# Optimization experiments

Hardware: AMD Instinct MI355X
Metric: run time of the kernel (lower is better)

## Reference

```python
import jax, jax.numpy as jnp
import numpy as np

B, L, D, H, NB = 8, 256, 128, 4, 2
HD = D // H
N_ITEMS, TIME_SPAN = 50000, 256
EPS = 1e-8
NEG = -(2.0 ** 32) + 1.0  # torch uses -2**32+1 padding value


def _ln(x, g, b):
    m = jnp.mean(x, -1, keepdims=True)
    v = jnp.mean((x - m) ** 2, -1, keepdims=True)
    return (x - m) / jnp.sqrt(v + EPS) * g + b


def setup_inputs() -> dict:
    ks = iter(jax.random.split(jax.random.key(0), 40))

    def nrm(shape, s=0.02):
        return jax.random.normal(next(ks), shape, jnp.float32) * s

    inp = {
        "user_ids": jax.random.randint(next(ks), (B,), 0, 1000),
        "log_seqs": jax.random.randint(next(ks), (B, L), 0, N_ITEMS + 1),
        "time_matrices": jax.random.randint(next(ks), (B, L, L), 0, TIME_SPAN + 1),
        "pos_seqs": jax.random.randint(next(ks), (B, L), 1, N_ITEMS + 1),
        "neg_seqs": jax.random.randint(next(ks), (B, L), 1, N_ITEMS + 1),
    }
    inp["item_emb"] = nrm((N_ITEMS + 1, D)).at[0].set(0.0)  # padding_idx=0
    inp["posK_emb"] = nrm((L, D))
    inp["posV_emb"] = nrm((L, D))
    inp["timeK_emb"] = nrm((TIME_SPAN + 1, D))
    inp["timeV_emb"] = nrm((TIME_SPAN + 1, D))
    inp["ln1_g"] = jnp.ones((NB, D)); inp["ln1_b"] = jnp.zeros((NB, D))
    inp["Wq"] = nrm((NB, D, D)); inp["bq"] = jnp.zeros((NB, D))
    inp["Wk"] = nrm((NB, D, D)); inp["bk"] = jnp.zeros((NB, D))
    inp["Wv"] = nrm((NB, D, D)); inp["bv"] = jnp.zeros((NB, D))
    inp["ln2_g"] = jnp.ones((NB, D)); inp["ln2_b"] = jnp.zeros((NB, D))
    inp["W1"] = nrm((NB, D, D)); inp["b1"] = jnp.zeros((NB, D))
    inp["W2"] = nrm((NB, D, D)); inp["b2"] = jnp.zeros((NB, D))
    inp["lnf_g"] = jnp.ones((D,)); inp["lnf_b"] = jnp.zeros((D,))
    return inp


def reference(user_ids, log_seqs, time_matrices, pos_seqs, neg_seqs,
              item_emb, posK_emb, posV_emb, timeK_emb, timeV_emb,
              ln1_g, ln1_b, Wq, bq, Wk, bk, Wv, bv, ln2_g, ln2_b,
              W1, b1, W2, b2, lnf_g, lnf_b):
    # dropout layers are identity in eval mode
    seqs = item_emb[log_seqs] * jnp.sqrt(jnp.float32(D))          # [B,L,D]
    tK = timeK_emb[time_matrices].reshape(B, L, L, H, HD)          # [B,Lq,Lk,H,hd]
    tV = timeV_emb[time_matrices].reshape(B, L, L, H, HD)
    pad = log_seqs == 0                                            # [B,L]
    seqs = seqs * (~pad)[..., None]
    causal = jnp.triu(jnp.ones((L, L), bool), 1)                   # ~tril -> masked
    # time_mask masks by QUERY position (matches torch unsqueeze(-1).expand)
    mask = pad[:, None, :, None] | causal[None, None]              # [B,1,Lq,Lk]
    posKh = posK_emb.reshape(L, H, HD)
    posVh = posV_emb.reshape(L, H, HD)
    for i in range(NB):
        q_in = _ln(seqs, ln1_g[i], ln1_b[i])
        Qh = (q_in @ Wq[i] + bq[i]).reshape(B, L, H, HD).transpose(0, 2, 1, 3)
        Kh = (seqs @ Wk[i] + bk[i]).reshape(B, L, H, HD).transpose(0, 2, 1, 3)
        Vh = (seqs @ Wv[i] + bv[i]).reshape(B, L, H, HD).transpose(0, 2, 1, 3)
        scores = jnp.einsum("bhqd,bhkd->bhqk", Qh, Kh)
        scores = scores + jnp.einsum("bhqd,khd->bhqk", Qh, posKh)
        scores = scores + jnp.einsum("bqkhd,bhqd->bhqk", tK, Qh)
        scores = scores / jnp.sqrt(jnp.float32(HD))
        scores = jnp.where(mask, NEG, scores)
        A = jax.nn.softmax(scores, axis=-1)                        # [B,H,Lq,Lk]
        out = jnp.einsum("bhqk,bhkd->bhqd", A, Vh)
        out = out + jnp.einsum("bhqk,khd->bhqd", A, posVh)
        out = out + jnp.einsum("bhqk,bqkhd->bhqd", A, tV)
        out = out.transpose(0, 2, 1, 3).reshape(B, L, D)
        seqs = q_in + out                                          # residual on Q
        seqs = _ln(seqs, ln2_g[i], ln2_b[i])
        h = jax.nn.relu(seqs @ W1[i] + b1[i])                      # conv1d k=1 == linear
        seqs = seqs + (h @ W2[i] + b2[i])
        seqs = seqs * (~pad)[..., None]
    feats = _ln(seqs, lnf_g, lnf_b)
    pos_logits = jnp.sum(feats * item_emb[pos_seqs], -1)           # [B,L]
    neg_logits = jnp.sum(feats * item_emb[neg_seqs], -1)
    return (pos_logits, neg_logits)
```

## Files before the change

kernel.cpp:

```cpp
#include <hip/hip_runtime.h>
#include <hip/hip_bf16.h>

#define L_ 256
#define H_ 4
#define ROWS 2048
#define NEGV (-4294967295.0f)

typedef unsigned short us16;

__device__ __forceinline__ float us2f(us16 u){ return __uint_as_float(((unsigned)u)<<16); }
__device__ __forceinline__ us16 f2us(float f){ __hip_bfloat16 h=__float2bfloat16(f); return *(us16*)&h; }

__device__ __forceinline__ float dot2bf(unsigned x, unsigned y, float c){
#if __has_builtin(__builtin_amdgcn_fdot2_f32_bf16)
    typedef __bf16 bf2 __attribute__((ext_vector_type(2)));
    union U{ unsigned u; bf2 v; };
    U ux, uy; ux.u=x; uy.u=y;
    return __builtin_amdgcn_fdot2_f32_bf16(ux.v, uy.v, c, false);
#else
    float r=fmaf(us2f((us16)(x&0xffffu)), us2f((us16)(y&0xffffu)), c);
    return fmaf(us2f((us16)(x>>16)), us2f((us16)(y>>16)), r);
#endif
}

struct KArgs {
    const int *log_seqs, *tmat, *pos_seqs, *neg_seqs;
    const float *item_emb, *posK, *posV, *timeK, *timeV;
    const float *ln1g, *ln1b, *bq, *bk, *bv, *ln2g, *ln2b, *b1, *b2, *lnfg, *lnfb;
    const float *Wq, *Wk, *Wv, *W1, *W2;
    float *qin0, *qin1, *out;
    unsigned *wsP;
    us16 *tmK, *tmV, *Qb0, *Kb0, *Vb0, *Qb1, *Kb1, *Vb1;
};

struct __align__(16) Smem {
    float    sS[8*256];
    float    sPr[16*128];
    float    sPj[2*257*4];
    unsigned sAb[8*128];
    int      sTM[512];
    unsigned sQb[128];
    float    sX[256];
    unsigned sXb[128];
    unsigned sHb[128];
    unsigned sYb[128];
    float    sRed[4], sRed2[4], sRB[8];
};

__device__ __forceinline__ float gemv128(const unsigned* __restrict__ wcol,
                                         const unsigned* __restrict__ xp){
    const uint4* w4=(const uint4*)wcol;
    const uint4* x4=(const uint4*)xp;
    float s0=0.f,s1=0.f,s2=0.f,s3=0.f;
    #pragma unroll
    for(int j=0;j<16;j++){
        uint4 w=w4[j], x=x4[j];
        s0=dot2bf(x.x,w.x,s0); s1=dot2bf(x.y,w.y,s1);
        s2=dot2bf(x.z,w.z,s2); s3=dot2bf(x.w,w.w,s3);
    }
    return (s0+s1)+(s2+s3);
}

__device__ __forceinline__ void ln_rows(float* sA,
        const float* __restrict__ g, const float* __restrict__ b,
        float* qin_out, int r0, int tid){
    int r=tid>>5, l=tid&31;
    float* x=sA+r*128;
    float x0=x[l],x1=x[l+32],x2=x[l+64],x3=x[l+96];
    float s=x0+x1+x2+x3;
    #pragma unroll
    for(int o=16;o;o>>=1) s+=__shfl_xor(s,o,64);
    float m=s*(1.f/128.f);
    float d0=x0-m,d1=x1-m,d2=x2-m,d3=x3-m;
    float v=d0*d0+d1*d1+d2*d2+d3*d3;
    #pragma unroll
    for(int o=16;o;o>>=1) v+=__shfl_xor(v,o,64);
    float rstd=rsqrtf(v*(1.f/128.f)+1e-8f);
    float y0=d0*rstd*g[l]+b[l];
    float y1=d1*rstd*g[l+32]+b[l+32];
    float y2=d2*rstd*g[l+64]+b[l+64];
    float y3=d3*rstd*g[l+96]+b[l+96];
    x[l]=y0; x[l+32]=y1; x[l+64]=y2; x[l+96]=y3;
    if(qin_out){
        float* q=qin_out+(size_t)(r0+r)*128;
        q[l]=y0; q[l+32]=y1; q[l+64]=y2; q[l+96]=y3;
    }
}

__global__ __launch_bounds__(256) void k_pre(KArgs a){
    __shared__ __align__(16) float sA[1024];
    int tid=threadIdx.x, bid=blockIdx.x;
    if(bid<768){
        int m=bid>>8, rg=bid&255, r0=rg*8;
        {
            int rl=tid>>5, c4=tid&31;
            int id=a.log_seqs[r0+rl];
            float4 v=((const float4*)a.item_emb)[id*32+c4];
            float sc = id? 11.3137085f : 0.f;
            v.x*=sc; v.y*=sc; v.z*=sc; v.w*=sc;
            ((float4*)sA)[tid]=v;
        }
        __syncthreads();
        if(m==0){ ln_rows(sA, a.ln1g, a.ln1b, a.qin0, r0, tid); __syncthreads(); }
        const float* Wsrc=(m==0)?a.Wq:(m==1)?a.Wk:a.Wv;
        int cp=tid&63, rp=tid>>6, c0=2*cp, ra=2*rp, rb=ra+1;
        float a00=0,a01=0,a10=0,a11=0;
        const float* Ar=sA+ra*128;
        const float* Br=sA+rb*128;
        #pragma unroll 8
        for(int kk=0;kk<128;kk++){
            float2 wp=((const float2*)(Wsrc+(size_t)kk*128))[cp];
            float x0=Ar[kk], x1=Br[kk];
            a00=fmaf(x0,wp.x,a00); a01=fmaf(x0,wp.y,a01);
            a10=fmaf(x1,wp.x,a10); a11=fmaf(x1,wp.y,a11);
        }
        int r_a=r0+ra, r_b=r0+rb;
        if(m==0){
            float b0v=a.bq[c0], b1v=a.bq[c0+1];
            ushort2 s0; s0.x=f2us(a00+b0v); s0.y=f2us(a01+b1v);
            ushort2 s1; s1.x=f2us(a10+b0v); s1.y=f2us(a11+b1v);
            *(ushort2*)(a.Qb0+(size_t)r_a*128+c0)=s0;
            *(ushort2*)(a.Qb0+(size_t)r_b*128+c0)=s1;
        } else if(m==1){
            float b0v=a.bk[c0], b1v=a.bk[c0+1];
            int qa=r_a&255, qb2=r_b&255;
            ushort2 s0; s0.x=f2us(a00+b0v+a.posK[qa*128+c0]);  s0.y=f2us(a01+b1v+a.posK[qa*128+c0+1]);
            ushort2 s1; s1.x=f2us(a10+b0v+a.posK[qb2*128+c0]); s1.y=f2us(a11+b1v+a.posK[qb2*128+c0+1]);
            *(ushort2*)(a.Kb0+(size_t)r_a*128+c0)=s0;
            *(ushort2*)(a.Kb0+(size_t)r_b*128+c0)=s1;
        } else {
            float b0v=a.bv[c0], b1v=a.bv[c0+1];
            int qa=r_a&255, qb2=r_b&255;
            unsigned lo0=f2us(a00+b0v+a.posV[qa*128+c0]);
            unsigned lo1=f2us(a01+b1v+a.posV[qa*128+c0+1]);
            unsigned hi0=f2us(a10+b0v+a.posV[qb2*128+c0]);
            unsigned hi1=f2us(a11+b1v+a.posV[qb2*128+c0+1]);
            unsigned* Vo=(unsigned*)a.Vb0+((size_t)r_a>>1)*128;
            Vo[c0]  =lo0|(hi0<<16);
            Vo[c0+1]=lo1|(hi1<<16);
        }
    } else if(bid<880){
        int j=bid-768; int m=j>>4; int sub=j&15;
        const float* base;
        switch(m){
            case 0: base=a.W1; break;        case 1: base=a.W2; break;
            case 2: base=a.Wq+16384; break;  case 3: base=a.Wk+16384; break;
            case 4: base=a.Wv+16384; break;  case 5: base=a.W1+16384; break;
            default: base=a.W2+16384; break;
        }
        unsigned* dst=a.wsP+(size_t)m*8192;
        #pragma unroll
        for(int t2=0;t2<2;t2++){
            int o=sub*512+t2*256+tid;
            int c=o>>6, kp=o&63;
            unsigned lo=f2us(base[(size_t)(2*kp)*128+c]);
            unsigned hi=f2us(base[(size_t)(2*kp+1)*128+c]);
            dst[o]=lo|(hi<<16);
        }
    } else {
        int gi=(bid-880)*256+tid;
        if(gi<8224){
            float4 v=((const float4*)a.timeK)[gi];
            ushort4 o; o.x=f2us(v.x);o.y=f2us(v.y);o.z=f2us(v.z);o.w=f2us(v.w);
            ((ushort4*)a.tmK)[gi]=o;
        } else if(gi<16448){
            int g2=gi-8224;
            float4 v=((const float4*)a.timeV)[g2];
            ushort4 o; o.x=f2us(v.x);o.y=f2us(v.y);o.z=f2us(v.z);o.w=f2us(v.w);
            ((ushort4*)a.tmV)[g2]=o;
        }
    }
}

__global__ __launch_bounds__(256,4) void k_blk(KArgs a, int layer){
    __shared__ Smem sm;
    int tid=threadIdx.x, bid=blockIdx.x;
    int b=bid>>7, p=bid&127;
    int q1=p, q2=255-p, b0=b*L_;
    int r1=b0+q1, r2=b0+q2;
    bool pad1=a.log_seqs[r1]==0, pad2=a.log_seqs[r2]==0;
    const us16* Qb = layer? a.Qb1:a.Qb0;
    const us16* Kb = layer? a.Kb1:a.Kb0;
    const unsigned* Vbu = (const unsigned*)(layer? a.Vb1:a.Vb0);
    const float* qin = layer? a.qin1:a.qin0;
    const float scale=0.17677669529663687f;

    if(tid<128){
        int rowq=tid>>6, j=tid&63;
        int r=rowq?r2:r1;
        sm.sQb[rowq*64+j]=((const unsigned*)Qb)[(size_t)r*64+j];
    }
    sm.sTM[tid]    =a.tmat[(size_t)r1*L_+tid];
    sm.sTM[256+tid]=a.tmat[(size_t)r2*L_+tid];
    __syncthreads();

    for(int t=tid;t<257;t+=256){
        const uint4* T4=(const uint4*)(a.tmK+(size_t)t*128);
        const uint4* Q40=(const uint4*)(sm.sQb);
        const uint4* Q41=(const uint4*)(sm.sQb+64);
        float4 p0v,p1v;
        float* pr0=&p0v.x; float* pr1=&p1v.x;
        #pragma unroll
        for(int h=0;h<4;h++){
            uint4 t0=T4[h*4+0],t1=T4[h*4+1],t2=T4[h*4+2],t3=T4[h*4+3];
            {
                uint4 qa=Q40[h*4+0],qb=Q40[h*4+1],qc=Q40[h*4+2],qd=Q40[h*4+3];
                float s0=0,s1=0;
                s0=dot2bf(qa.x,t0.x,s0); s1=dot2bf(qa.y,t0.y,s1);
                s0=dot2bf(qa.z,t0.z,s0); s1=dot2bf(qa.w,t0.w,s1);
                s0=dot2bf(qb.x,t1.x,s0); s1=dot2bf(qb.y,t1.y,s1);
                s0=dot2bf(qb.z,t1.z,s0); s1=dot2bf(qb.w,t1.w,s1);
                s0=dot2bf(qc.x,t2.x,s0); s1=dot2bf(qc.y,t2.y,s1);
                s0=dot2bf(qc.z,t2.z,s0); s1=dot2bf(qc.w,t2.w,s1);
                s0=dot2bf(qd.x,t3.x,s0); s1=dot2bf(qd.y,t3.y,s1);
                s0=dot2bf(qd.z,t3.z,s0); s1=dot2bf(qd.w,t3.w,s1);
                pr0[h]=s0+s1;
            }
            {
                uint4 qa=Q41[h*4+0],qb=Q41[h*4+1],qc=Q41[h*4+2],qd=Q41[h*4+3];
                float s0=0,s1=0;
                s0=dot2bf(qa.x,t0.x,s0); s1=dot2bf(qa.y,t0.y,s1);
                s0=dot2bf(qa.z,t0.z,s0); s1=dot2bf(qa.w,t0.w,s1);
                s0=dot2bf(qb.x,t1.x,s0); s1=dot2bf(qb.y,t1.y,s1);
                s0=dot2bf(qb.z,t1.z,s0); s1=dot2bf(qb.w,t1.w,s1);
                s0=dot2bf(qc.x,t2.x,s0); s1=dot2bf(qc.y,t2.y,s1);
                s0=dot2bf(qc.z,t2.z,s0); s1=dot2bf(qc.w,t2.w,s1);
                s0=dot2bf(qd.x,t3.x,s0); s1=dot2bf(qd.y,t3.y,s1);
                s0=dot2bf(qd.z,t3.z,s0); s1=dot2bf(qd.w,t3.w,s1);
                pr1[h]=s0+s1;
            }
        }
        ((float4*)sm.sPj)[t]    =p0v;
        ((float4*)sm.sPj)[257+t]=p1v;
    }
    __syncthreads();

    {
        int k=tid;
        const uint4* K4=(const uint4*)(Kb+(size_t)(b0+k)*128);
        #pragma unroll
        for(int i2=0;i2<2;i2++){
            int qq=i2?q2:q1; bool pad=i2?pad2:pad1;
            int tm=sm.sTM[i2*256+k];
            bool act=(k<=qq)&&!pad;
            float o0=NEGV,o1=NEGV,o2=NEGV,o3=NEGV;
            if(act){
                const uint4* Q4=(const uint4*)(sm.sQb+i2*64);
                float4 pj=((const float4*)sm.sPj)[i2*257+tm];
                float r4[4];
                #pragma unroll
                for(int h=0;h<4;h++){
                    uint4 k0=K4[h*4+0],k1=K4[h*4+1],k2=K4[h*4+2],k3=K4[h*4+3];
                    uint4 qa=Q4[h*4+0],qb=Q4[h*4+1],qc=Q4[h*4+2],qd=Q4[h*4+3];
                    float s0=0,s1=0;
                    s0=dot2bf(qa.x,k0.x,s0); s1=dot2bf(qa.y,k0.y,s1);
                    s0=dot2bf(qa.z,k0.z,s0); s1=dot2bf(qa.w,k0.w,s1);
                    s0=dot2bf(qb.x,k1.x,s0); s1=dot2bf(qb.y,k1.y,s1);
                    s0=dot2bf(qb.z,k1.z,s0); s1=dot2bf(qb.w,k1.w,s1);
                    s0=dot2bf(qc.x,k2.x,s0); s1=dot2bf(qc.y,k2.y,s1);
                    s0=dot2bf(qc.z,k2.z,s0); s1=dot2bf(qc.w,k2.w,s1);
                    s0=dot2bf(qd.x,k3.x,s0); s1=dot2bf(qd.y,k3.y,s1);
                    s0=dot2bf(qd.z,k3.z,s0); s1=dot2bf(qd.w,k3.w,s1);
                    r4[h]=s0+s1;
                }
                o0=(r4[0]+pj.x)*scale; o1=(r4[1]+pj.y)*scale;
                o2=(r4[2]+pj.z)*scale; o3=(r4[3]+pj.w)*scale;
            }
            sm.sS[(i2*4+0)*256+k]=o0; sm.sS[(i2*4+1)*256+k]=o1;
            sm.sS[(i2*4+2)*256+k]=o2; sm.sS[(i2*4+3)*256+k]=o3;
        }
    }
    __syncthreads();

    {
        int h=tid>>6, lane=tid&63;
        us16* sab=(us16*)sm.sAb;
        #pragma unroll
        for(int i2=0;i2<2;i2++){
            const float* row=sm.sS+(i2*4+h)*256;
            float v0=row[lane],v1=row[lane+64],v2=row[lane+128],v3=row[lane+192];
            float mm=fmaxf(fmaxf(v0,v1),fmaxf(v2,v3));
            #pragma unroll
            for(int o=32;o;o>>=1) mm=fmaxf(mm,__shfl_xor(mm,o,64));
            float e0=__expf(v0-mm),e1=__expf(v1-mm),e2=__expf(v2-mm),e3=__expf(v3-mm);
            float ss=e0+e1+e2+e3;
            #pragma unroll
            for(int o=32;o;o>>=1) ss+=__shfl_xor(ss,o,64);
            float inv=1.f/ss;
            us16* ar=sab+(i2*4+h)*256;
            ar[lane]    =f2us(e0*inv); ar[lane+64] =f2us(e1*inv);
            ar[lane+128]=f2us(e2*inv); ar[lane+192]=f2us(e3*inv);
        }
    }
    __syncthreads();

    {
        int i2=tid>>7, s8=(tid>>4)&7, dq=tid&15;
        int qq=i2?q2:q1; bool pad=i2?pad2:pad1;
        int kend=pad?L_:qq+1;
        int k0=s8*32;
        int kmax=kend-k0; kmax=kmax<0?0:(kmax>32?32:kmax);
        int npair=(kmax+1)>>1;
        const unsigned* arow=sm.sAb+(i2*4+(dq>>2))*128;
        const int* tmrow=sm.sTM+i2*256;
        float ac0=0,ac1=0,ac2=0,ac3=0,ac4=0,ac5=0,ac6=0,ac7=0;
        for(int kp=0;kp<npair;kp++){
            int kx=k0+2*kp;
            unsigned aa=arow[kx>>1];
            int tma=tmrow[kx], tmb=tmrow[kx+1];
            const uint4* Vp=(const uint4*)(Vbu+((size_t)(b0+kx)>>1)*128+dq*8);
            uint4 va=Vp[0], vb4=Vp[1];
            uint4 ta=((const uint4*)(a.tmV+(size_t)tma*128))[dq];
            uint4 tb=((const uint4*)(a.tmV+(size_t)tmb*128))[dq];
            ac0=dot2bf(aa,va.x,ac0);  ac1=dot2bf(aa,va.y,ac1);
            ac2=dot2bf(aa,va.z,ac2);  ac3=dot2bf(aa,va.w,ac3);
            ac4=dot2bf(aa,vb4.x,ac4); ac5=dot2bf(aa,vb4.y,ac5);
            ac6=dot2bf(aa,vb4.z,ac6); ac7=dot2bf(aa,vb4.w,ac7);
            unsigned p0=__builtin_amdgcn_perm(tb.x,ta.x,0x05040100u);
            unsigned p1=__builtin_amdgcn_perm(tb.x,ta.x,0x07060302u);
            unsigned p2=__builtin_amdgcn_perm(tb.y,ta.y,0x05040100u);
            unsigned p3=__builtin_amdgcn_perm(tb.y,ta.y,0x07060302u);
            unsigned p4=__builtin_amdgcn_perm(tb.z,ta.z,0x05040100u);
            unsigned p5=__builtin_amdgcn_perm(tb.z,ta.z,0x07060302u);
            unsigned p6=__builtin_amdgcn_perm(tb.w,ta.w,0x05040100u);
            unsigned p7=__builtin_amdgcn_perm(tb.w,ta.w,0x07060302u);
            ac0=dot2bf(aa,p0,ac0); ac1=dot2bf(aa,p1,ac1);
            ac2=dot2bf(aa,p2,ac2); ac3=dot2bf(aa,p3,ac3);
            ac4=dot2bf(aa,p4,ac4); ac5=dot2bf(aa,p5,ac5);
            ac6=dot2bf(aa,p6,ac6); ac7=dot2bf(aa,p7,ac7);
        }
        float* dst=sm.sPr+(i2*8+s8)*128+dq*8;
        ((float4*)dst)[0]=make_float4(ac0,ac1,ac2,ac3);
        ((float4*)dst)[1]=make_float4(ac4,ac5,ac6,ac7);
    }
    __syncthreads();

    int ii=tid>>7, l=tid&127;
    bool padown = ii? pad2:pad1;
    int rr = ii? r2:r1;
    int qown = ii? q2:q1;
    {
        float v=qin[(size_t)rr*128+l];
        #pragma unroll
        for(int sl=0;sl<8;sl++) v+=sm.sPr[(ii*8+sl)*128+l];
        float s=v;
        #pragma unroll
        for(int o=32;o;o>>=1) s+=__shfl_xor(s,o,64);
        if((tid&63)==0) sm.sRed[ii*2+((tid>>6)&1)]=s;
        __syncthreads();
        float m=(sm.sRed[ii*2]+sm.sRed[ii*2+1])*(1.f/128.f);
        float d=v-m;
        float vv=d*d;
        #pragma unroll
        for(int o=32;o;o>>=1) vv+=__shfl_xor(vv,o,64);
        if((tid&63)==0) sm.sRed2[ii*2+((tid>>6)&1)]=vv;
        __syncthreads();
        float rstd=rsqrtf((sm.sRed2[ii*2]+sm.sRed2[ii*2+1])*(1.f/128.f)+1e-8f);
        float y=d*rstd*a.ln2g[layer*128+l]+a.ln2b[layer*128+l];
        sm.sX[ii*128+l]=y;
        ((us16*)sm.sXb)[ii*128+l]=f2us(y);
    }
    __syncthreads();

    int cc=l;
    {
        float h1=gemv128(a.wsP+(size_t)(layer?5:0)*8192+(size_t)cc*64, sm.sXb+ii*64);
        h1=fmaxf(h1+a.b1[layer*128+cc],0.f);
        ((us16*)sm.sHb)[ii*128+cc]=f2us(h1);
    }
    __syncthreads();
    float f;
    {
        f=gemv128(a.wsP+(size_t)(layer?6:1)*8192+(size_t)cc*64, sm.sHb+ii*64)
          +a.b2[layer*128+cc]+sm.sX[ii*128+cc];
        if(padown) f=0.f;
    }

    if(layer==0){
        ((us16*)sm.sYb)[ii*128+cc]=f2us(f);
        float s=f;
        #pragma unroll
        for(int o=32;o;o>>=1) s+=__shfl_xor(s,o,64);
        if((tid&63)==0) sm.sRB[ii*2+((tid>>6)&1)]=s;
        __syncthreads();
        float m=(sm.sRB[ii*2]+sm.sRB[ii*2+1])*(1.f/128.f);
        float d=f-m;
        float vv=d*d;
        #pragma unroll
        for(int o=32;o;o>>=1) vv+=__shfl_xor(vv,o,64);
        if((tid&63)==0) sm.sRB[4+ii*2+((tid>>6)&1)]=vv;
        __syncthreads();
        float rstd=rsqrtf((sm.sRB[4+ii*2]+sm.sRB[5+ii*2])*(1.f/128.f)+1e-8f);
        float y1=d*rstd*a.ln1g[128+cc]+a.ln1b[128+cc];
        a.qin1[(size_t)rr*128+cc]=y1;
        ((us16*)sm.sXb)[ii*128+cc]=f2us(y1);
        __syncthreads();
        float accq=gemv128(a.wsP+(size_t)2*8192+(size_t)cc*64, sm.sXb+ii*64)+a.bq[128+cc];
        a.Qb1[(size_t)rr*128+cc]=f2us(accq);
        float acck=gemv128(a.wsP+(size_t)3*8192+(size_t)cc*64, sm.sYb+ii*64)+a.bk[128+cc]+a.posK[qown*128+cc];
        a.Kb1[(size_t)rr*128+cc]=f2us(acck);
        float accv=gemv128(a.wsP+(size_t)4*8192+(size_t)cc*64, sm.sYb+ii*64)+a.bv[128+cc]+a.posV[qown*128+cc];
        ((us16*)a.Vb1)[((size_t)rr>>1)*256+2*cc+(rr&1)]=f2us(accv);
    } else {
        float s=f;
        #pragma unroll
        for(int o=32;o;o>>=1) s+=__shfl_xor(s,o,64);
        if((tid&63)==0) sm.sRB[ii*2+((tid>>6)&1)]=s;
        __syncthreads();
        float m=(sm.sRB[ii*2]+sm.sRB[ii*2+1])*(1.f/128.f);
        float d=f-m;
        float vv=d*d;
        #pragma unroll
        for(int o=32;o;o>>=1) vv+=__shfl_xor(vv,o,64);
        if((tid&63)==0) sm.sRB[4+ii*2+((tid>>6)&1)]=vv;
        __syncthreads();
        float rstd=rsqrtf((sm.sRB[4+ii*2]+sm.sRB[5+ii*2])*(1.f/128.f)+1e-8f);
        sm.sX[ii*128+cc]=d*rstd*a.lnfg[cc]+a.lnfb[cc];
        __syncthreads();
        int w=tid>>6, lane=tid&63;
        int rowi=w>>1, neg=w&1;
        int rg = rowi? r2:r1;
        int id = neg? a.neg_seqs[rg] : a.pos_seqs[rg];
        const float* e=a.item_emb+(size_t)id*128;
        float s2 = sm.sX[rowi*128+lane]*e[lane] + sm.sX[rowi*128+lane+64]*e[lane+64];
        #pragma unroll
        for(int o=32;o;o>>=1) s2+=__shfl_xor(s2,o,64);
        if(lane==0) a.out[neg*ROWS+rg]=s2;
    }
}

extern "C" void kernel_launch(void* const* d_in, const int* in_sizes, int n_in,
                              void* d_out, int out_size, void* d_ws, size_t ws_size,
                              hipStream_t stream) {
    KArgs a;
    a.log_seqs=(const int*)d_in[1];
    a.tmat    =(const int*)d_in[2];
    a.pos_seqs=(const int*)d_in[3];
    a.neg_seqs=(const int*)d_in[4];
    a.item_emb=(const float*)d_in[5];
    a.posK =(const float*)d_in[6];
    a.posV =(const float*)d_in[7];
    a.timeK=(const float*)d_in[8];
    a.timeV=(const float*)d_in[9];
    a.ln1g=(const float*)d_in[10];
    a.ln1b=(const float*)d_in[11];
    a.Wq=(const float*)d_in[12];
    a.bq=(const float*)d_in[13];
    a.Wk=(const float*)d_in[14];
    a.bk=(const float*)d_in[15];
    a.Wv=(const float*)d_in[16];
    a.bv=(const float*)d_in[17];
    a.ln2g=(const float*)d_in[18];
    a.ln2b=(const float*)d_in[19];
    a.W1=(const float*)d_in[20];
    a.b1=(const float*)d_in[21];
    a.W2=(const float*)d_in[22];
    a.b2=(const float*)d_in[23];
    a.lnfg=(const float*)d_in[24];
    a.lnfb=(const float*)d_in[25];

    const size_t MB=1u<<20;
    char* w=(char*)d_ws;
    a.qin0=(float*)(w+0*MB);
    a.qin1=(float*)(w+1*MB);
    a.Qb0 =(us16*) (w+2*MB);
    a.Kb0 =(us16*) (w+2*MB+512*1024);
    a.Vb0 =(us16*) (w+3*MB);
    a.Qb1 =(us16*) (w+3*MB+512*1024);
    a.Kb1 =(us16*) (w+4*MB);
    a.Vb1 =(us16*) (w+4*MB+512*1024);
    a.wsP =(unsigned*)(w+5*MB);
    a.tmK =(us16*) (w+5*MB+256*1024);
    a.tmV =(us16*) (w+5*MB+384*1024);
    a.out =(float*)d_out;

    k_pre<<<946,256,0,stream>>>(a);
    k_blk<<<1024,256,0,stream>>>(a,0);
    k_blk<<<1024,256,0,stream>>>(a,1);
}
```

Measured before the change: 234.7 us.

## Transpose packed weight layout for coalesced GEMV and split time-key projection across lanes

```diff
diff --git a/kernel.cpp b/kernel.cpp
--- a/kernel.cpp
+++ b/kernel.cpp
@@ -47,18 +47,15 @@
     float    sRed[4], sRed2[4], sRB[8];
 };
 
-__device__ __forceinline__ float gemv128(const unsigned* __restrict__ wcol,
-                                         const unsigned* __restrict__ xp){
-    const uint4* w4=(const uint4*)wcol;
-    const uint4* x4=(const uint4*)xp;
-    float s0=0.f,s1=0.f,s2=0.f,s3=0.f;
-    #pragma unroll
-    for(int j=0;j<16;j++){
-        uint4 w=w4[j], x=x4[j];
-        s0=dot2bf(x.x,w.x,s0); s1=dot2bf(x.y,w.y,s1);
-        s2=dot2bf(x.z,w.z,s2); s3=dot2bf(x.w,w.w,s3);
-    }
-    return (s0+s1)+(s2+s3);
+__device__ __forceinline__ float gemv128(const unsigned* __restrict__ wp,
+                                         const unsigned* __restrict__ xp, int c){
+    float s0=0.f, s1=0.f;
+    #pragma unroll 8
+    for(int kp=0;kp<64;kp+=2){
+        s0=dot2bf(xp[kp],   wp[kp*128+c],     s0);
+        s1=dot2bf(xp[kp+1], wp[(kp+1)*128+c], s1);
+    }
+    return s0+s1;
 }
 
 __device__ __forceinline__ void ln_rows(float* sA,
@@ -152,7 +149,7 @@
         #pragma unroll
         for(int t2=0;t2<2;t2++){
             int o=sub*512+t2*256+tid;
-            int c=o>>6, kp=o&63;
+            int kp=o>>7, c=o&127;
             unsigned lo=f2us(base[(size_t)(2*kp)*128+c]);
             unsigned hi=f2us(base[(size_t)(2*kp+1)*128+c]);
             dst[o]=lo|(hi<<16);
@@ -194,44 +191,25 @@
     sm.sTM[256+tid]=a.tmat[(size_t)r2*L_+tid];
     __syncthreads();
 
-    for(int t=tid;t<257;t+=256){
-        const uint4* T4=(const uint4*)(a.tmK+(size_t)t*128);
-        const uint4* Q40=(const uint4*)(sm.sQb);
-        const uint4* Q41=(const uint4*)(sm.sQb+64);
-        float4 p0v,p1v;
-        float* pr0=&p0v.x; float* pr1=&p1v.x;
-        #pragma unroll
-        for(int h=0;h<4;h++){
-            uint4 t0=T4[h*4+0],t1=T4[h*4+1],t2=T4[h*4+2],t3=T4[h*4+3];
-            {
-                uint4 qa=Q40[h*4+0],qb=Q40[h*4+1],qc=Q40[h*4+2],qd=Q40[h*4+3];
-                float s0=0,s1=0;
-                s0=dot2bf(qa.x,t0.x,s0); s1=dot2bf(qa.y,t0.y,s1);
-                s0=dot2bf(qa.z,t0.z,s0); s1=dot2bf(qa.w,t0.w,s1);
-                s0=dot2bf(qb.x,t1.x,s0); s1=dot2bf(qb.y,t1.y,s1);
-                s0=dot2bf(qb.z,t1.z,s0); s1=dot2bf(qb.w,t1.w,s1);
-                s0=dot2bf(qc.x,t2.x,s0); s1=dot2bf(qc.y,t2.y,s1);
-                s0=dot2bf(qc.z,t2.z,s0); s1=dot2bf(qc.w,t2.w,s1);
-                s0=dot2bf(qd.x,t3.x,s0); s1=dot2bf(qd.y,t3.y,s1);
-                s0=dot2bf(qd.z,t3.z,s0); s1=dot2bf(qd.w,t3.w,s1);
-                pr0[h]=s0+s1;
+    {
+        int ch=tid&15;
+        int h=ch>>2;
+        uint4 qv0=((const uint4*)(sm.sQb))[ch];
+        uint4 qv1=((const uint4*)(sm.sQb+64))[ch];
+        for(int t=tid>>4; t<257; t+=16){
+            uint4 tv=((const uint4*)(a.tmK+(size_t)t*128))[ch];
+            float p0=0.f,p1=0.f;
+            p0=dot2bf(qv0.x,tv.x,p0); p0=dot2bf(qv0.y,tv.y,p0);
+            p0=dot2bf(qv0.z,tv.z,p0); p0=dot2bf(qv0.w,tv.w,p0);
+            p1=dot2bf(qv1.x,tv.x,p1); p1=dot2bf(qv1.y,tv.y,p1);
+            p1=dot2bf(qv1.z,tv.z,p1); p1=dot2bf(qv1.w,tv.w,p1);
+            p0+=__shfl_xor(p0,1,64); p0+=__shfl_xor(p0,2,64);
+            p1+=__shfl_xor(p1,1,64); p1+=__shfl_xor(p1,2,64);
+            if((ch&3)==0){
+                sm.sPj[t*4+h]        =p0;
+                sm.sPj[257*4+t*4+h]  =p1;
             }
-            {
-                uint4 qa=Q41[h*4+0],qb=Q41[h*4+1],qc=Q41[h*4+2],qd=Q41[h*4+3];
-                float s0=0,s1=0;
-                s0=dot2bf(qa.x,t0.x,s0); s1=dot2bf(qa.y,t0.y,s1);
-                s0=dot2bf(qa.z,t0.z,s0); s1=dot2bf(qa.w,t0.w,s1);
-                s0=dot2bf(qb.x,t1.x,s0); s1=dot2bf(qb.y,t1.y,s1);
-                s0=dot2bf(qb.z,t1.z,s0); s1=dot2bf(qb.w,t1.w,s1);
-                s0=dot2bf(qc.x,t2.x,s0); s1=dot2bf(qc.y,t2.y,s1);
-                s0=dot2bf(qc.z,t2.z,s0); s1=dot2bf(qc.w,t2.w,s1);
-                s0=dot2bf(qd.x,t3.x,s0); s1=dot2bf(qd.y,t3.y,s1);
-                s0=dot2bf(qd.z,t3.z,s0); s1=dot2bf(qd.w,t3.w,s1);
-                pr1[h]=s0+s1;
-            }
-        }
-        ((float4*)sm.sPj)[t]    =p0v;
-        ((float4*)sm.sPj)[257+t]=p1v;
+        }
     }
     __syncthreads();
 
@@ -364,14 +342,14 @@
 
     int cc=l;
     {
-        float h1=gemv128(a.wsP+(size_t)(layer?5:0)*8192+(size_t)cc*64, sm.sXb+ii*64);
+        float h1=gemv128(a.wsP+(size_t)(layer?5:0)*8192, sm.sXb+ii*64, cc);
         h1=fmaxf(h1+a.b1[layer*128+cc],0.f);
         ((us16*)sm.sHb)[ii*128+cc]=f2us(h1);
     }
     __syncthreads();
     float f;
     {
-        f=gemv128(a.wsP+(size_t)(layer?6:1)*8192+(size_t)cc*64, sm.sHb+ii*64)
+        f=gemv128(a.wsP+(size_t)(layer?6:1)*8192, sm.sHb+ii*64, cc)
           +a.b2[layer*128+cc]+sm.sX[ii*128+cc];
         if(padown) f=0.f;
     }
@@ -395,11 +373,11 @@
         a.qin1[(size_t)rr*128+cc]=y1;
         ((us16*)sm.sXb)[ii*128+cc]=f2us(y1);
         __syncthreads();
-        float accq=gemv128(a.wsP+(size_t)2*8192+(size_t)cc*64, sm.sXb+ii*64)+a.bq[128+cc];
+        float accq=gemv128(a.wsP+(size_t)2*8192, sm.sXb+ii*64, cc)+a.bq[128+cc];
         a.Qb1[(size_t)rr*128+cc]=f2us(accq);
-        float acck=gemv128(a.wsP+(size_t)3*8192+(size_t)cc*64, sm.sYb+ii*64)+a.bk[128+cc]+a.posK[qown*128+cc];
+        float acck=gemv128(a.wsP+(size_t)3*8192, sm.sYb+ii*64, cc)+a.bk[128+cc]+a.posK[qown*128+cc];
         a.Kb1[(size_t)rr*128+cc]=f2us(acck);
-        float accv=gemv128(a.wsP+(size_t)4*8192+(size_t)cc*64, sm.sYb+ii*64)+a.bv[128+cc]+a.posV[qown*128+cc];
+        float accv=gemv128(a.wsP+(size_t)4*8192, sm.sYb+ii*64, cc)+a.bv[128+cc]+a.posV[qown*128+cc];
         ((us16*)a.Vb1)[((size_t)rr>>1)*256+2*cc+(rr&1)]=f2us(accv);
     } else {
         float s=f;
```

Measured after the change: 195.7 us. -16.6%, faster.
